# Kernel tuning notes

Hardware: AMD Instinct MI355X
Metric: run time of the kernel (lower is better)

Reference implementation:

```python
import jax, jax.numpy as jnp
import numpy as np

V, E, H, N, B, T_CAP = 10000, 2048, 512, 98, 32, 61


def setup_inputs() -> dict:
    key = jax.random.key(0)
    ks = jax.random.split(key, 24)
    p = lambda k, shape: jax.random.normal(k, shape, dtype=jnp.float32) * 0.02
    inp = {
        "img_features": jax.random.normal(ks[0], (B, N, E), dtype=jnp.float32),
        "captions": jax.random.randint(ks[1], (B, T_CAP), 0, V),
        "emb": p(ks[2], (V, H)),
        "W_init_h": p(ks[3], (H, E)), "b_init_h": jnp.zeros((H,), jnp.float32),
        "W_init_c": p(ks[4], (H, E)), "b_init_c": jnp.zeros((H,), jnp.float32),
        "W_U": p(ks[5], (H, H)), "b_U": jnp.zeros((H,), jnp.float32),
        "W_att": p(ks[6], (H, E)), "b_att": jnp.zeros((H,), jnp.float32),
        "W_v": p(ks[7], (1, H)), "b_v": jnp.zeros((1,), jnp.float32),
        "W_fb": p(ks[8], (E, H)), "b_fb": jnp.zeros((E,), jnp.float32),
        "W_ih": p(ks[9], (4 * H, H + E)), "b_ih": jnp.zeros((4 * H,), jnp.float32),
        "W_hh": p(ks[10], (4 * H, H)), "b_hh": jnp.zeros((4 * H,), jnp.float32),
        "W_out": p(ks[11], (V, H)), "b_out": jnp.zeros((V,), jnp.float32),
    }
    return inp


def reference(img_features, captions, emb, W_init_h, b_init_h, W_init_c, b_init_c,
              W_U, b_U, W_att, b_att, W_v, b_v, W_fb, b_fb,
              W_ih, b_ih, W_hh, b_hh, W_out, b_out):
    # training-mode forward: max_timespan = caption_len - 1; dropout as identity (eval-style determinism)
    T = captions.shape[1] - 1
    avg = img_features.mean(axis=1)  # [B, E]
    h = jnp.tanh(avg @ W_init_h.T + b_init_h)  # [B, H]
    c = jnp.tanh(avg @ W_init_c.T + b_init_c)
    # Embeddings with sqrt(d_model) scaling
    emb_seq = emb[captions] * jnp.sqrt(jnp.float32(emb.shape[1]))  # [B, T_cap, H]
    # W_s is timestep-invariant: hoist out of loop (same math)
    Ws = jnp.einsum('bne,he->bnh', img_features, W_att) + b_att  # [B, N, H]

    def step(carry, emb_t):
        h, c = carry
        att = jnp.tanh(Ws + (h @ W_U.T + b_U)[:, None, :])       # [B, N, H]
        e = jnp.einsum('bnh,h->bn', att, W_v[0]) + b_v[0]        # [B, N]
        alpha = jax.nn.softmax(e, axis=1)
        context = jnp.einsum('bne,bn->be', img_features, alpha)  # [B, E]
        gate = jax.nn.sigmoid(h @ W_fb.T + b_fb)                 # [B, E]
        x = jnp.concatenate([emb_t, gate * context], axis=1)     # [B, H+E]
        gates = x @ W_ih.T + b_ih + h @ W_hh.T + b_hh            # [B, 4H]
        i_, f_, g_, o_ = jnp.split(gates, 4, axis=1)             # torch LSTMCell gate order
        c2 = jax.nn.sigmoid(f_) * c + jax.nn.sigmoid(i_) * jnp.tanh(g_)
        h2 = jax.nn.sigmoid(o_) * jnp.tanh(c2)
        pred = h2 @ W_out.T + b_out                              # [B, V]
        return (h2, c2), pred

    emb_steps = jnp.swapaxes(emb_seq[:, :T], 0, 1)  # [T, B, H]
    (_, _), preds = jax.lax.scan(step, (h, c), emb_steps)
    return jnp.swapaxes(preds, 0, 1)  # [B, T, V]
```

## Files before the change

kernel.cpp:

```cpp
#include <hip/hip_runtime.h>
#include <hip/hip_bf16.h>

#define BB   32
#define NN   98
#define EE   2048
#define HH   512
#define VV   10000
#define TT   60
#define TCAP 61
#define NBLK 256
#define FLG  512

typedef unsigned short u16;
typedef unsigned long long u64;
typedef __attribute__((ext_vector_type(8))) short bh8;
typedef __attribute__((ext_vector_type(4))) float f32x4;

__device__ __forceinline__ float bsf(unsigned s) {
    union { unsigned u; float f; } w; w.u = s << 16; return w.f;
}
__device__ __forceinline__ u16 f2bu(float f) {
    union { float f; unsigned u; } v; v.f = f;
    unsigned u = v.u;
    u = u + 0x7fffu + ((u >> 16) & 1u);
    return (u16)(u >> 16);
}
__device__ __forceinline__ bh8 ld8(const u16* p) {
    return *reinterpret_cast<const bh8*>(p);
}
__device__ __forceinline__ float sigm(float x) {
    return __builtin_amdgcn_rcpf(1.0f + exp2f(-1.4426950408889634f * x));
}
__device__ __forceinline__ float tanh_(float x) {
    return 1.0f - 2.0f * __builtin_amdgcn_rcpf(1.0f + exp2f(2.885390081777927f * x));
}

__device__ __forceinline__ void stf_coh(float* p, float v) {
    __hip_atomic_store(p, v, __ATOMIC_RELAXED, __HIP_MEMORY_SCOPE_AGENT);
}
__device__ __forceinline__ void stu16_coh(u16* p, u16 v) {
    __hip_atomic_store(p, v, __ATOMIC_RELAXED, __HIP_MEMORY_SCOPE_AGENT);
}
__device__ __forceinline__ void stu32_coh(unsigned* p, unsigned v) {
    __hip_atomic_store(p, v, __ATOMIC_RELAXED, __HIP_MEMORY_SCOPE_AGENT);
}
__device__ __forceinline__ unsigned ldu32_coh(const unsigned* p) {
    return __hip_atomic_load(p, __ATOMIC_RELAXED, __HIP_MEMORY_SCOPE_AGENT);
}

__global__ __launch_bounds__(256) void k_conv_all(
    const float* __restrict__ s_img, const float* __restrict__ s_watt,
    const float* __restrict__ s_winh, const float* __restrict__ s_winc,
    const float* __restrict__ s_wu,  const float* __restrict__ s_wfb,
    const float* __restrict__ s_wih, const float* __restrict__ s_whh,
    const float* __restrict__ s_wout, u16* __restrict__ dst)
{
    size_t i = (size_t)blockIdx.x * 256 + threadIdx.x;
    size_t e = i * 4;
    const float* src; size_t off;
    if      (e <  6422528) { src = s_img;  off = 0; }
    else if (e <  7471104) { src = s_watt; off = 6422528; }
    else if (e <  8519680) { src = s_winh; off = 7471104; }
    else if (e <  9568256) { src = s_winc; off = 8519680; }
    else if (e <  9830400) { src = s_wu;   off = 9568256; }
    else if (e < 10878976) { src = s_wfb;  off = 9830400; }
    else if (e < 16121856) { src = s_wih;  off = 10878976; }
    else if (e < 17170432) { src = s_whh;  off = 16121856; }
    else                   { src = s_wout; off = 17170432; }
    float4 v = reinterpret_cast<const float4*>(src)[(e - off) >> 2];
    ushort4 o;
    o.x = f2bu(v.x); o.y = f2bu(v.y); o.z = f2bu(v.z); o.w = f2bu(v.w);
    reinterpret_cast<ushort4*>(dst)[i] = o;
}

__global__ __launch_bounds__(256) void k_init1(
    const float* __restrict__ img, const int* __restrict__ caps,
    const float* __restrict__ emb, u16* __restrict__ avg_bf, u16* __restrict__ emb_all)
{
    int bid = blockIdx.x, tid = threadIdx.x;
    if (bid < 256) {
        int b = bid >> 3, et = bid & 7;
        int ec = et * 256 + tid;
        const float* p = img + (size_t)(b * NN) * EE + ec;
        float s = 0.f;
        for (int n = 0; n < NN; ++n) s += p[(size_t)n * EE];
        avg_bf[b * EE + ec] = f2bu(s * (1.0f / 98.0f));
    } else {
        int eb = bid - 256;
        for (int r8 = 0; r8 < 8; ++r8) {
            int row = eb * 8 + r8;
            int t = row >> 5, b = row & 31;
            int cap = caps[b * TCAP + t];
            const float* src = emb + (size_t)cap * HH;
            u16* dst = emb_all + (size_t)row * HH;
            for (int c = tid; c < HH; c += 256)
                dst[c] = f2bu(src[c] * 22.627416997969522f);
        }
    }
}

__global__ __launch_bounds__(256) void k_init2(
    const u16* __restrict__ avg_bf,
    const u16* __restrict__ Wh_bf, const float* __restrict__ b_h,
    const u16* __restrict__ Wc_bf, const float* __restrict__ b_c,
    u16* __restrict__ h_all, float* __restrict__ c_ws)
{
    __shared__ float red[4][2][64][4];
    int ot = blockIdx.x, tid = threadIdx.x;
    int w = tid >> 6, lane = tid & 63, quad = lane >> 4, l16 = lane & 15;
    int o = ot * 16 + l16;
    const u16* wrow = (o < HH) ? (Wh_bf + (size_t)o * EE) : (Wc_bf + (size_t)(o - HH) * EE);
    f32x4 acc[2]; acc[0] = {0,0,0,0}; acc[1] = {0,0,0,0};
    for (int c = w * 16; c < w * 16 + 16; ++c) {
        int k = c * 32 + quad * 8;
        bh8 b8 = ld8(wrow + k);
        for (int mt = 0; mt < 2; ++mt) {
            bh8 a8 = ld8(avg_bf + (size_t)(mt * 16 + l16) * EE + k);
            acc[mt] = __builtin_amdgcn_mfma_f32_16x16x32_bf16(a8, b8, acc[mt], 0, 0, 0);
        }
    }
    for (int mt = 0; mt < 2; ++mt)
        for (int r = 0; r < 4; ++r) red[w][mt][lane][r] = acc[mt][r];
    __syncthreads();
    for (int idx = tid; idx < 512; idx += 256) {
        int mg = idx >> 4, nn2 = idx & 15;
        int mt = mg >> 4, m = mg & 15;
        int sl = nn2 + 16 * (m >> 2), rg = m & 3;
        float v = red[0][mt][sl][rg] + red[1][mt][sl][rg] + red[2][mt][sl][rg] + red[3][mt][sl][rg];
        int oo = ot * 16 + nn2, b = mg;
        if (oo < HH)
            h_all[(size_t)b * HH + oo] = f2bu(tanh_(v + b_h[oo]));
        else
            c_ws[b * HH + (oo - HH)] = tanh_(v + b_c[oo - HH]);
    }
}

__global__ __launch_bounds__(256) void k_ws(
    const u16* __restrict__ img_bf, const u16* __restrict__ Watt_bf,
    const float* __restrict__ b_att, u16* __restrict__ Ws_bf)
{
    int bid = blockIdx.x, tid = threadIdx.x;
    int mt = bid >> 4, nt = bid & 15;
    int w = tid >> 6, lane = tid & 63, quad = lane >> 4, l16 = lane & 15;
    int rowA = mt * 64 + w * 16 + l16;
    f32x4 acc[2]; acc[0] = {0,0,0,0}; acc[1] = {0,0,0,0};
    const u16* arow = img_bf + (size_t)rowA * EE;
    for (int c = 0; c < 64; ++c) {
        int k = c * 32 + quad * 8;
        bh8 a8 = ld8(arow + k);
        for (int s = 0; s < 2; ++s) {
            bh8 b8 = ld8(Watt_bf + (size_t)(nt * 32 + s * 16 + l16) * EE + k);
            acc[s] = __builtin_amdgcn_mfma_f32_16x16x32_bf16(a8, b8, acc[s], 0, 0, 0);
        }
    }
    for (int s = 0; s < 2; ++s)
        for (int r = 0; r < 4; ++r) {
            int m = quad * 4 + r;
            int row = mt * 64 + w * 16 + m;
            int col = nt * 32 + s * 16 + l16;
            Ws_bf[(size_t)row * HH + col] = f2bu(acc[s][r] + b_att[col]);
        }
}

__global__ void k_zero(unsigned* cnt) {
    int t = threadIdx.x;
    for (int i = 0; i < 36; ++i) stu32_coh(&cnt[t + i * 256], 0u);
}

__device__ __forceinline__ void gsync(unsigned* cnt, unsigned epoch) {
    __syncthreads();
    const int tid = threadIdx.x, bid = blockIdx.x;
    if (bid == 0) {
        if (tid == 0) stu32_coh(&cnt[0], epoch);
        const u64* p = reinterpret_cast<const u64*>(cnt) + tid;
        for (;;) {
            bool ok = true;
            if (tid < 128) {
                u64 v = __hip_atomic_load(p, __ATOMIC_RELAXED, __HIP_MEMORY_SCOPE_AGENT);
                ok = ((unsigned)v >= epoch) && ((unsigned)(v >> 32) >= epoch);
            }
            if (__syncthreads_and(ok)) break;
            __builtin_amdgcn_s_sleep(1);
        }
        stu32_coh(&cnt[FLG + tid * 32], epoch);
        __syncthreads();
    } else {
        if (tid == 0) {
            stu32_coh(&cnt[bid], epoch);
            while (ldu32_coh(&cnt[FLG + bid * 32]) < epoch)
                __builtin_amdgcn_s_sleep(2);
        }
        __syncthreads();
    }
}

__global__ __launch_bounds__(256, 2) void k_loop(
    const u16* __restrict__ img_bf,
    const u16* __restrict__ Ws_bf,
    float* __restrict__ Wu_all, float* __restrict__ gate_all,
    const float* __restrict__ W_v, const float* __restrict__ b_v,
    u16* __restrict__ xctx_all,
    const u16* __restrict__ emb_all,
    u16* __restrict__ h_all,
    const u16* __restrict__ Wih_bf, const float* __restrict__ b_ih,
    const u16* __restrict__ Whh_bf, const float* __restrict__ b_hh,
    float* __restrict__ c_ws,
    const u16* __restrict__ WU_bf, const float* __restrict__ b_U,
    const u16* __restrict__ Wfb_bf, const float* __restrict__ b_fb,
    unsigned* cnt)
{
    __shared__ float redC[4][2][64][9];
    __shared__ float redB[4][64][17];
    __shared__ float wu_sh[HH];
    __shared__ float part[2][128][3];
    __shared__ float e_sh[NN];
    __shared__ float a_sh[NN];

    const int bid = blockIdx.x, tid = threadIdx.x;
    const int w = tid >> 6, lane = tid & 63, quad = lane >> 4, l16 = lane & 15;
    unsigned snc = 0;

    auto phaseC = [&](int tIn) {
        if (bid < 80) {
            int ot = bid;
            const u16* wrow[2];
            #pragma unroll
            for (int s = 0; s < 2; ++s) {
                int o = ot * 32 + s * 16 + l16;
                wrow[s] = (o < HH) ? (WU_bf + (size_t)o * HH)
                                   : (Wfb_bf + (size_t)(o - HH) * HH);
            }
            const u16* hbase = h_all + (size_t)tIn * BB * HH;
            f32x4 acc[2][2];
            for (int mt = 0; mt < 2; ++mt) for (int s = 0; s < 2; ++s) acc[mt][s] = {0,0,0,0};
            for (int c = w * 4; c < w * 4 + 4; ++c) {
                int k = c * 32 + quad * 8;
                bh8 b8[2];
                #pragma unroll
                for (int s = 0; s < 2; ++s) b8[s] = ld8(wrow[s] + k);
                #pragma unroll
                for (int mt = 0; mt < 2; ++mt) {
                    bh8 a8 = ld8(hbase + (size_t)(mt * 16 + l16) * HH + k);
                    #pragma unroll
                    for (int s = 0; s < 2; ++s)
                        acc[mt][s] = __builtin_amdgcn_mfma_f32_16x16x32_bf16(a8, b8[s], acc[mt][s], 0, 0, 0);
                }
            }
            for (int mt = 0; mt < 2; ++mt)
                for (int s = 0; s < 2; ++s)
                    for (int r = 0; r < 4; ++r) redC[w][mt][lane][s * 4 + r] = acc[mt][s][r];
            __syncthreads();
            for (int idx = tid; idx < 1024; idx += 256) {
                int b = idx & 31, col = idx >> 5;
                int s = col >> 4, nn = col & 15;
                int mt = b >> 4, m = b & 15;
                int sl = (m >> 2) * 16 + nn, rg = s * 4 + (m & 3);
                float v = redC[0][mt][sl][rg] + redC[1][mt][sl][rg]
                        + redC[2][mt][sl][rg] + redC[3][mt][sl][rg];
                int o = ot * 32 + col;
                if (o < HH)
                    stf_coh(&Wu_all[((size_t)tIn * BB + b) * HH + o], v + b_U[o]);
                else
                    stf_coh(&gate_all[((size_t)tIn * BB + b) * EE + (o - HH)], sigm(v + b_fb[o - HH]));
            }
        }
    };

    auto phaseA = [&](int t) {
        int b = bid & 31, s8 = bid >> 5;
        const float* wubase = Wu_all + ((size_t)t * BB + b) * HH;
        {
            float2 t2 = *reinterpret_cast<const float2*>(wubase + tid * 2);
            wu_sh[tid * 2] = t2.x; wu_sh[tid * 2 + 1] = t2.y;
        }
        __syncthreads();
        float wu[8], wv[8];
        #pragma unroll
        for (int j = 0; j < 8; ++j) { wu[j] = wu_sh[lane * 8 + j]; wv[j] = W_v[lane * 8 + j]; }
        for (int n = w; n < NN; n += 4) {
            bh8 ws8 = ld8(Ws_bf + (size_t)(b * NN + n) * HH + lane * 8);
            float acc = 0.f;
            #pragma unroll
            for (int j = 0; j < 8; ++j) acc += wv[j] * tanh_(bsf((u16)ws8[j]) + wu[j]);
            #pragma unroll
            for (int off = 32; off > 0; off >>= 1) acc += __shfl_down(acc, off, 64);
            if (lane == 0) e_sh[n] = acc + b_v[0];
        }
        __syncthreads();
        if (tid < 64) {
            float e0 = e_sh[tid];
            float e1 = (tid + 64 < NN) ? e_sh[tid + 64] : -1e30f;
            float m = fmaxf(e0, e1);
            #pragma unroll
            for (int off = 32; off > 0; off >>= 1) m = fmaxf(m, __shfl_xor(m, off, 64));
            const float L2E = 1.4426950408889634f;
            float x0 = exp2f((e0 - m) * L2E);
            float x1 = (tid + 64 < NN) ? exp2f((e1 - m) * L2E) : 0.f;
            float s = x0 + x1;
            #pragma unroll
            for (int off = 32; off > 0; off >>= 1) s += __shfl_xor(s, off, 64);
            float inv = __builtin_amdgcn_rcpf(s);
            a_sh[tid] = x0 * inv;
            if (tid + 64 < NN) a_sh[tid + 64] = x1 * inv;
        }
        __syncthreads();
        int pc = tid & 127, nq = tid >> 7;
        int c0 = s8 * 256 + pc * 2;
        int n0 = nq * 49, n1 = n0 + 49;
        float a0 = 0.f, a1 = 0.f;
        for (int n = n0; n < n1; ++n) {
            unsigned u = *reinterpret_cast<const unsigned*>(img_bf + (size_t)(b * NN + n) * EE + c0);
            float a = a_sh[n];
            a0 = fmaf(a, bsf(u & 0xffffu), a0);
            a1 = fmaf(a, bsf(u >> 16), a1);
        }
        part[nq][pc][0] = a0; part[nq][pc][1] = a1;
        __syncthreads();
        if (tid < 128) {
            float C0 = part[0][tid][0] + part[1][tid][0];
            float C1 = part[0][tid][1] + part[1][tid][1];
            int ec = s8 * 256 + tid * 2;
            float2 g = *reinterpret_cast<const float2*>(
                gate_all + ((size_t)t * BB + b) * EE + ec);
            unsigned outw = ((unsigned)f2bu(g.y * C1) << 16) | (unsigned)f2bu(g.x * C0);
            stu32_coh(reinterpret_cast<unsigned*>(
                xctx_all + ((size_t)t * BB + b) * EE + ec), outw);
        }
    };

    auto phaseB = [&](int t) {
        if (bid < 64) {
            int kt = bid & 31, mt = bid >> 5;
            int brow = mt * 16 + l16;
            const u16* embrow = emb_all + (size_t)(t * BB + brow) * HH;
            const u16* xrow   = xctx_all + ((size_t)t * BB + brow) * EE;
            const u16* hrow   = h_all + (size_t)(t * BB + brow) * HH;
            const u16* wihp[4]; const u16* whhp[4];
            #pragma unroll
            for (int jt = 0; jt < 4; ++jt) {
                int j = kt * 16 + jt * 4 + (l16 & 3) + HH * (l16 >> 2);
                wihp[jt] = Wih_bf + (size_t)j * (HH + EE);
                whhp[jt] = Whh_bf + (size_t)j * HH;
            }
            f32x4 acc[4];
            #pragma unroll
            for (int jt = 0; jt < 4; ++jt) acc[jt] = {0,0,0,0};
            for (int c = w * 24; c < w * 24 + 24; ++c) {
                int k = c * 32 + quad * 8;
                bh8 a8;
                if (c < 16)      a8 = ld8(embrow + k);
                else if (c < 80) a8 = ld8(xrow + (k - HH));
                else             a8 = ld8(hrow + (k - HH - EE));
                #pragma unroll
                for (int jt = 0; jt < 4; ++jt) {
                    bh8 b8 = (c < 80) ? ld8(wihp[jt] + k) : ld8(whhp[jt] + (k - HH - EE));
                    acc[jt] = __builtin_amdgcn_mfma_f32_16x16x32_bf16(a8, b8, acc[jt], 0, 0, 0);
                }
            }
            for (int jt = 0; jt < 4; ++jt)
                for (int r = 0; r < 4; ++r) redB[w][lane][jt * 4 + r] = acc[jt][r];
            __syncthreads();
            {
                int m = tid >> 4, kk = tid & 15;
                float g4[4];
                #pragma unroll
                for (int g = 0; g < 4; ++g) {
                    int nn = (kk & 3) | (g << 2);
                    int jt = kk >> 2;
                    int sl = (m >> 2) * 16 + nn, rg = m & 3;
                    int jj = kt * 16 + kk + HH * g;
                    g4[g] = redB[0][sl][jt * 4 + rg] + redB[1][sl][jt * 4 + rg]
                          + redB[2][sl][jt * 4 + rg] + redB[3][sl][jt * 4 + rg]
                          + b_ih[jj] + b_hh[jj];
                }
                int b = mt * 16 + m, k = kt * 16 + kk;
                float cold = c_ws[b * HH + k];
                float c2 = sigm(g4[1]) * cold + sigm(g4[0]) * tanh_(g4[2]);
                float h2 = sigm(g4[3]) * tanh_(c2);
                c_ws[b * HH + k] = c2;
                stu16_coh(&h_all[(size_t)((t + 1) * BB + b) * HH + k], f2bu(h2));
            }
        }
    };

    phaseC(0);
    gsync(cnt, ++snc);
    for (int t = 0; t < TT; ++t) {
        phaseA(t);
        gsync(cnt, ++snc);
        phaseB(t);
        gsync(cnt, ++snc);
        if (t < TT - 1) {
            phaseC(t + 1);
            gsync(cnt, ++snc);
        }
    }
}

__global__ __launch_bounds__(256) void k_pred(
    const u16* __restrict__ h_all, const u16* __restrict__ Wout_bf,
    const float* __restrict__ b_out, float* __restrict__ out)
{
    int bid = blockIdx.x, tid = threadIdx.x;
    int mt = bid / 79, vt = bid % 79;
    int w = tid >> 6, lane = tid & 63, quad = lane >> 4, l16 = lane & 15;
    f32x4 acc[8][2];
    for (int mi = 0; mi < 8; ++mi) for (int s = 0; s < 2; ++s) acc[mi][s] = {0,0,0,0};
    int nact[2]; int vbase[2];
    for (int s = 0; s < 2; ++s) {
        int ntg = vt * 8 + 2 * w + s;
        nact[s] = (ntg < 625);
        vbase[s] = ntg * 16;
    }
    for (int c = 0; c < 16; ++c) {
        int k = c * 32 + quad * 8;
        bh8 b8[2];
        for (int s = 0; s < 2; ++s) if (nact[s])
            b8[s] = ld8(Wout_bf + (size_t)(vbase[s] + l16) * HH + k);
        for (int mi = 0; mi < 8; ++mi) {
            int row = 32 + mt * 128 + mi * 16 + l16;
            bh8 a8 = ld8(h_all + (size_t)row * HH + k);
            for (int s = 0; s < 2; ++s) if (nact[s])
                acc[mi][s] = __builtin_amdgcn_mfma_f32_16x16x32_bf16(a8, b8[s], acc[mi][s], 0, 0, 0);
        }
    }
    for (int s = 0; s < 2; ++s) if (nact[s]) {
        int v = vbase[s] + l16;
        float bo = b_out[v];
        for (int mi = 0; mi < 8; ++mi)
            for (int r = 0; r < 4; ++r) {
                int row = 32 + mt * 128 + mi * 16 + quad * 4 + r;
                int tt = (row >> 5) - 1, b = row & 31;
                out[(size_t)(b * TT + tt) * VV + v] = acc[mi][s][r] + bo;
            }
    }
}

extern "C" void kernel_launch(void* const* d_in, const int* in_sizes, int n_in,
                              void* d_out, int out_size, void* d_ws, size_t ws_size,
                              hipStream_t stream)
{
    const float* img      = (const float*)d_in[0];
    const int*   caps     = (const int*)d_in[1];
    const float* emb      = (const float*)d_in[2];
    const float* W_init_h = (const float*)d_in[3];
    const float* b_init_h = (const float*)d_in[4];
    const float* W_init_c = (const float*)d_in[5];
    const float* b_init_c = (const float*)d_in[6];
    const float* W_U      = (const float*)d_in[7];
    const float* b_U      = (const float*)d_in[8];
    const float* W_att    = (const float*)d_in[9];
    const float* b_att    = (const float*)d_in[10];
    const float* W_v      = (const float*)d_in[11];
    const float* b_v      = (const float*)d_in[12];
    const float* W_fb     = (const float*)d_in[13];
    const float* b_fb     = (const float*)d_in[14];
    const float* W_ih     = (const float*)d_in[15];
    const float* b_ih     = (const float*)d_in[16];
    const float* W_hh     = (const float*)d_in[17];
    const float* b_hh     = (const float*)d_in[18];
    const float* W_out    = (const float*)d_in[19];
    const float* b_out    = (const float*)d_in[20];
    float* out = (float*)d_out;

    char* ws = (char*)d_ws;
    u16*   img_bf   = (u16*)(ws);
    u16*   Watt_bf  = (u16*)(ws + 12845056);
    u16*   Winh_bf  = (u16*)(ws + 14942208);
    u16*   Winc_bf  = (u16*)(ws + 17039360);
    u16*   WU_bf    = (u16*)(ws + 19136512);
    u16*   Wfb_bf   = (u16*)(ws + 19660800);
    u16*   Wih_bf   = (u16*)(ws + 21757952);
    u16*   Whh_bf   = (u16*)(ws + 32243712);
    u16*   Wout_bf  = (u16*)(ws + 34340864);
    u16*   Ws_bf    = (u16*)(ws + 44580864);
    u16*   emb_all  = (u16*)(ws + 47792128);
    u16*   h_all    = (u16*)(ws + 49758208);
    u16*   avg_bf   = (u16*)(ws + 51757056);
    float* c_ws     = (float*)(ws + 51888128);
    u16*   xctx_all = (u16*)(ws + 51953664);
    float* Wu_all   = (float*)(ws + 59949056);
    float* gate_all = (float*)(ws + 63946752);
    unsigned* sync_cnt = (unsigned*)avg_bf;

    k_conv_all<<<21768, 256, 0, stream>>>(img, W_att, W_init_h, W_init_c, W_U,
                                          W_fb, W_ih, W_hh, W_out, img_bf);

    k_init1<<<496, 256, 0, stream>>>(img, caps, emb, avg_bf, emb_all);
    k_init2<<<64, 256, 0, stream>>>(avg_bf, Winh_bf, b_init_h, Winc_bf, b_init_c, h_all, c_ws);
    k_ws<<<784, 256, 0, stream>>>(img_bf, Watt_bf, b_att, Ws_bf);

    k_zero<<<1, 256, 0, stream>>>(sync_cnt);
    k_loop<<<NBLK, 256, 0, stream>>>(img_bf, Ws_bf, Wu_all, gate_all, W_v, b_v, xctx_all,
                                     emb_all, h_all, Wih_bf, b_ih, Whh_bf, b_hh, c_ws,
                                     WU_bf, b_U, Wfb_bf, b_fb, sync_cnt);

    k_pred<<<1185, 256, 0, stream>>>(h_all, Wout_bf, b_out, out);
}
```

Before: 2.945 ms.

## Use 512-thread blocks in recurrent loop and reuse W_out tiles in prediction

The persistent recurrent kernel now runs 512 threads per block, splitting the K-dimension reductions, attention rows and context sum across 8 warps instead of 4, with shared reduction buffers unioned. The aim is to shorten each latency-bound timestep. The prediction GEMM is regridded to 240 blocks that each loop over 5 M-tiles, reusing W_out columns and cutting block count. The larger blocks tighten the register budget and add reduction overhead.

```diff
diff --git a/kernel.cpp b/kernel.cpp
--- a/kernel.cpp
+++ b/kernel.cpp
@@ -182,7 +182,7 @@
             if (__syncthreads_and(ok)) break;
             __builtin_amdgcn_s_sleep(1);
         }
-        stu32_coh(&cnt[FLG + tid * 32], epoch);
+        if (tid < 256) stu32_coh(&cnt[FLG + tid * 32], epoch);
         __syncthreads();
     } else {
         if (tid == 0) {
@@ -194,7 +194,7 @@
     }
 }
 
-__global__ __launch_bounds__(256, 2) void k_loop(
+__global__ __launch_bounds__(512, 2) void k_loop(
     const u16* __restrict__ img_bf,
     const u16* __restrict__ Ws_bf,
     float* __restrict__ Wu_all, float* __restrict__ gate_all,
@@ -209,10 +209,12 @@
     const u16* __restrict__ Wfb_bf, const float* __restrict__ b_fb,
     unsigned* cnt)
 {
-    __shared__ float redC[4][2][64][9];
-    __shared__ float redB[4][64][17];
+    __shared__ union {
+        float C[8][2][64][9];
+        float B[8][64][17];
+    } red;
     __shared__ float wu_sh[HH];
-    __shared__ float part[2][128][3];
+    __shared__ float part[4][128][3];
     __shared__ float e_sh[NN];
     __shared__ float a_sh[NN];
 
@@ -233,7 +235,7 @@
             const u16* hbase = h_all + (size_t)tIn * BB * HH;
             f32x4 acc[2][2];
             for (int mt = 0; mt < 2; ++mt) for (int s = 0; s < 2; ++s) acc[mt][s] = {0,0,0,0};
-            for (int c = w * 4; c < w * 4 + 4; ++c) {
+            for (int c = w * 2; c < w * 2 + 2; ++c) {
                 int k = c * 32 + quad * 8;
                 bh8 b8[2];
                 #pragma unroll
@@ -248,15 +250,17 @@
             }
             for (int mt = 0; mt < 2; ++mt)
                 for (int s = 0; s < 2; ++s)
-                    for (int r = 0; r < 4; ++r) redC[w][mt][lane][s * 4 + r] = acc[mt][s][r];
+                    for (int r = 0; r < 4; ++r) red.C[w][mt][lane][s * 4 + r] = acc[mt][s][r];
             __syncthreads();
-            for (int idx = tid; idx < 1024; idx += 256) {
+            for (int idx = tid; idx < 1024; idx += 512) {
                 int b = idx & 31, col = idx >> 5;
                 int s = col >> 4, nn = col & 15;
                 int mt = b >> 4, m = b & 15;
                 int sl = (m >> 2) * 16 + nn, rg = s * 4 + (m & 3);
-                float v = redC[0][mt][sl][rg] + redC[1][mt][sl][rg]
-                        + redC[2][mt][sl][rg] + redC[3][mt][sl][rg];
+                float v = red.C[0][mt][sl][rg] + red.C[1][mt][sl][rg]
+                        + red.C[2][mt][sl][rg] + red.C[3][mt][sl][rg]
+                        + red.C[4][mt][sl][rg] + red.C[5][mt][sl][rg]
+                        + red.C[6][mt][sl][rg] + red.C[7][mt][sl][rg];
                 int o = ot * 32 + col;
                 if (o < HH)
                     stf_coh(&Wu_all[((size_t)tIn * BB + b) * HH + o], v + b_U[o]);
@@ -269,15 +273,12 @@
     auto phaseA = [&](int t) {
         int b = bid & 31, s8 = bid >> 5;
         const float* wubase = Wu_all + ((size_t)t * BB + b) * HH;
-        {
-            float2 t2 = *reinterpret_cast<const float2*>(wubase + tid * 2);
-            wu_sh[tid * 2] = t2.x; wu_sh[tid * 2 + 1] = t2.y;
-        }
+        wu_sh[tid] = wubase[tid];
         __syncthreads();
         float wu[8], wv[8];
         #pragma unroll
         for (int j = 0; j < 8; ++j) { wu[j] = wu_sh[lane * 8 + j]; wv[j] = W_v[lane * 8 + j]; }
-        for (int n = w; n < NN; n += 4) {
+        for (int n = w; n < NN; n += 8) {
             bh8 ws8 = ld8(Ws_bf + (size_t)(b * NN + n) * HH + lane * 8);
             float acc = 0.f;
             #pragma unroll
@@ -306,7 +307,7 @@
         __syncthreads();
         int pc = tid & 127, nq = tid >> 7;
         int c0 = s8 * 256 + pc * 2;
-        int n0 = nq * 49, n1 = n0 + 49;
+        int n0 = nq * 25, n1 = (nq == 3) ? NN : n0 + 25;
         float a0 = 0.f, a1 = 0.f;
         for (int n = n0; n < n1; ++n) {
             unsigned u = *reinterpret_cast<const unsigned*>(img_bf + (size_t)(b * NN + n) * EE + c0);
@@ -317,8 +318,8 @@
         part[nq][pc][0] = a0; part[nq][pc][1] = a1;
         __syncthreads();
         if (tid < 128) {
-            float C0 = part[0][tid][0] + part[1][tid][0];
-            float C1 = part[0][tid][1] + part[1][tid][1];
+            float C0 = part[0][tid][0] + part[1][tid][0] + part[2][tid][0] + part[3][tid][0];
+            float C1 = part[0][tid][1] + part[1][tid][1] + part[2][tid][1] + part[3][tid][1];
             int ec = s8 * 256 + tid * 2;
             float2 g = *reinterpret_cast<const float2*>(
                 gate_all + ((size_t)t * BB + b) * EE + ec);
@@ -345,7 +346,7 @@
             f32x4 acc[4];
             #pragma unroll
             for (int jt = 0; jt < 4; ++jt) acc[jt] = {0,0,0,0};
-            for (int c = w * 24; c < w * 24 + 24; ++c) {
+            for (int c = w * 12; c < w * 12 + 12; ++c) {
                 int k = c * 32 + quad * 8;
                 bh8 a8;
                 if (c < 16)      a8 = ld8(embrow + k);
@@ -358,9 +359,9 @@
                 }
             }
             for (int jt = 0; jt < 4; ++jt)
-                for (int r = 0; r < 4; ++r) redB[w][lane][jt * 4 + r] = acc[jt][r];
+                for (int r = 0; r < 4; ++r) red.B[w][lane][jt * 4 + r] = acc[jt][r];
             __syncthreads();
-            {
+            if (tid < 256) {
                 int m = tid >> 4, kk = tid & 15;
                 float g4[4];
                 #pragma unroll
@@ -369,9 +370,10 @@
                     int jt = kk >> 2;
                     int sl = (m >> 2) * 16 + nn, rg = m & 3;
                     int jj = kt * 16 + kk + HH * g;
-                    g4[g] = redB[0][sl][jt * 4 + rg] + redB[1][sl][jt * 4 + rg]
-                          + redB[2][sl][jt * 4 + rg] + redB[3][sl][jt * 4 + rg]
-                          + b_ih[jj] + b_hh[jj];
+                    float v = b_ih[jj] + b_hh[jj];
+                    #pragma unroll
+                    for (int ww = 0; ww < 8; ++ww) v += red.B[ww][sl][jt * 4 + rg];
+                    g4[g] = v;
                 }
                 int b = mt * 16 + m, k = kt * 16 + kk;
                 float cold = c_ws[b * HH + k];
@@ -402,37 +404,43 @@
     const float* __restrict__ b_out, float* __restrict__ out)
 {
     int bid = blockIdx.x, tid = threadIdx.x;
-    int mt = bid / 79, vt = bid % 79;
+    int r8 = bid & 7, m8 = bid >> 3;
+    int q = m8 / 3, ck = m8 % 3;
+    int vt = q * 8 + r8;
+    if (vt >= 79) return;
     int w = tid >> 6, lane = tid & 63, quad = lane >> 4, l16 = lane & 15;
-    f32x4 acc[8][2];
-    for (int mi = 0; mi < 8; ++mi) for (int s = 0; s < 2; ++s) acc[mi][s] = {0,0,0,0};
     int nact[2]; int vbase[2];
     for (int s = 0; s < 2; ++s) {
         int ntg = vt * 8 + 2 * w + s;
         nact[s] = (ntg < 625);
         vbase[s] = ntg * 16;
     }
-    for (int c = 0; c < 16; ++c) {
-        int k = c * 32 + quad * 8;
-        bh8 b8[2];
-        for (int s = 0; s < 2; ++s) if (nact[s])
-            b8[s] = ld8(Wout_bf + (size_t)(vbase[s] + l16) * HH + k);
-        for (int mi = 0; mi < 8; ++mi) {
-            int row = 32 + mt * 128 + mi * 16 + l16;
-            bh8 a8 = ld8(h_all + (size_t)row * HH + k);
+    float bo[2];
+    for (int s = 0; s < 2; ++s) bo[s] = nact[s] ? b_out[vbase[s] + l16] : 0.f;
+    for (int mt = ck * 5; mt < ck * 5 + 5; ++mt) {
+        f32x4 acc[8][2];
+        for (int mi = 0; mi < 8; ++mi) for (int s = 0; s < 2; ++s) acc[mi][s] = {0,0,0,0};
+        for (int c = 0; c < 16; ++c) {
+            int k = c * 32 + quad * 8;
+            bh8 b8[2];
             for (int s = 0; s < 2; ++s) if (nact[s])
-                acc[mi][s] = __builtin_amdgcn_mfma_f32_16x16x32_bf16(a8, b8[s], acc[mi][s], 0, 0, 0);
-        }
-    }
-    for (int s = 0; s < 2; ++s) if (nact[s]) {
-        int v = vbase[s] + l16;
-        float bo = b_out[v];
-        for (int mi = 0; mi < 8; ++mi)
-            for (int r = 0; r < 4; ++r) {
-                int row = 32 + mt * 128 + mi * 16 + quad * 4 + r;
-                int tt = (row >> 5) - 1, b = row & 31;
-                out[(size_t)(b * TT + tt) * VV + v] = acc[mi][s][r] + bo;
-            }
+                b8[s] = ld8(Wout_bf + (size_t)(vbase[s] + l16) * HH + k);
+            for (int mi = 0; mi < 8; ++mi) {
+                int row = 32 + mt * 128 + mi * 16 + l16;
+                bh8 a8 = ld8(h_all + (size_t)row * HH + k);
+                for (int s = 0; s < 2; ++s) if (nact[s])
+                    acc[mi][s] = __builtin_amdgcn_mfma_f32_16x16x32_bf16(a8, b8[s], acc[mi][s], 0, 0, 0);
+            }
+        }
+        for (int s = 0; s < 2; ++s) if (nact[s]) {
+            int v = vbase[s] + l16;
+            for (int mi = 0; mi < 8; ++mi)
+                for (int r = 0; r < 4; ++r) {
+                    int row = 32 + mt * 128 + mi * 16 + quad * 4 + r;
+                    int tt = (row >> 5) - 1, b = row & 31;
+                    out[(size_t)(b * TT + tt) * VV + v] = acc[mi][s][r] + bo[s];
+                }
+        }
     }
 }
 
@@ -491,9 +499,9 @@
     k_ws<<<784, 256, 0, stream>>>(img_bf, Watt_bf, b_att, Ws_bf);
 
     k_zero<<<1, 256, 0, stream>>>(sync_cnt);
-    k_loop<<<NBLK, 256, 0, stream>>>(img_bf, Ws_bf, Wu_all, gate_all, W_v, b_v, xctx_all,
+    k_loop<<<NBLK, 512, 0, stream>>>(img_bf, Ws_bf, Wu_all, gate_all, W_v, b_v, xctx_all,
                                      emb_all, h_all, Wih_bf, b_ih, Whh_bf, b_hh, c_ws,
                                      WU_bf, b_U, Wfb_bf, b_fb, sync_cnt);
 
-    k_pred<<<1185, 256, 0, stream>>>(h_all, Wout_bf, b_out, out);
-}
+    k_pred<<<240, 256, 0, stream>>>(h_all, Wout_bf, b_out, out);
+}
```

Result: no change. 2.972 ms (+0.9%).
